# Optimization experiments

Measured on AMD Instinct MI355X. Metric: run time of the kernel, lower is better.

The kernel has to match this reference:

```python
import jax, jax.numpy as jnp
import numpy as np
import math

B, N, D = 4096, 41, 271
S, THR, KS = 0.3, 1e-4, 25  # wavelet scale s=0.3, threshold 1e-4, Bessel series terms
_IV_COEFS = [np.array([1.0 / (math.factorial(k) * math.factorial(k + n)) for k in range(KS)], dtype=np.float32) for n in range(4)]


def _iv(n, x):
    # modified Bessel I_n(x) via power series, x >= 0, shape [B]
    k = np.arange(KS, dtype=np.float32)
    xh = (0.5 * x)[:, None]
    return jnp.sum(_IV_COEFS[n] * xh ** (n + 2.0 * k), axis=-1)


def _l1norm(W):
    # F.normalize(p=1, dim=2)
    return W / jnp.maximum(jnp.sum(jnp.abs(W), axis=2, keepdims=True), 1e-12)


def _bn(x, g, b):
    # BatchNorm1d in training mode: per-feature stats over the batch dim (biased var)
    m = jnp.mean(x, 0)
    v = jnp.var(x, 0)
    return (x - m) / jnp.sqrt(v + 1e-5) * g + b


def _wavelet_basis(G):
    # laplacian_multi: degree from raw W, symmetrize, D^-1/2 (D - A) D^-1/2
    deg = jnp.sum(G, axis=-1)                               # [B,N]
    A = 0.5 * (G + jnp.swapaxes(G, 1, 2))                   # [B,N,N]
    dinv = 1.0 / (jnp.sqrt(deg) + 1e-6)
    eye = jnp.eye(N, dtype=G.dtype)
    L = dinv[:, :, None] * (deg[:, :, None] * eye - A) * dinv[:, None, :]
    # cheb_polynomial_multi: note order-0 term is ZEROS in the source
    T2 = 2.0 * jnp.matmul(L, L)
    T3 = 2.0 * jnp.matmul(L, T2) - L
    Lch = jnp.stack([jnp.zeros_like(L), L, T2, T3], axis=1)  # [B,4,N,N]
    # largest_lamb: host-side eigsh(LM) per sample -> detached (no grad)
    lam = jax.lax.stop_gradient(jnp.max(jnp.abs(jnp.linalg.eigvalsh(L)), axis=-1))  # [B]
    x = S * 0.5 * lam                                       # s * a, a = lamb/2
    ivs = jnp.stack([_iv(n, x) for n in range(4)], axis=1)  # [B,4]
    sign = jnp.asarray([1.0, -1.0, 1.0, -1.0], dtype=x.dtype)  # I_n(-x) = (-1)^n I_n(x)
    c = 2.0 * jnp.exp(x)[:, None] * ivs                     # 2 e^{sa} I_n(sa)
    inv_c = 2.0 * jnp.exp(-x)[:, None] * ivs * sign         # 2 e^{-sa} I_n(-sa)
    W = jnp.einsum('bo,bonm->bnm', c, Lch)
    Wi = jnp.einsum('bo,bonm->bnm', inv_c, Lch)
    W = _l1norm(jnp.where(W < THR, 0.0, W))
    Wi = _l1norm(jnp.where(Wi < THR, 0.0, Wi))
    return W, Wi


def _forward(G, X, gwnn_kernel, gwnn_W, log_scale_vector, W1, b1, W2, b2, bn1_gamma, bn1_beta):
    wav, wav_inv = _wavelet_basis(G)
    # graph wavelet layer: psi diag(k) psi^{-1} X W  (dropout off / eval)
    h = jnp.matmul(X, gwnn_W)                 # [B,N,D]
    h = jnp.matmul(wav_inv, h)
    h = gwnn_kernel[None, :, None] * h
    h = jax.nn.relu(jnp.matmul(wav, h))
    # scaling layer: exp(log_scale) * x
    coff = jnp.exp(log_scale_vector)          # [N,D]
    fr = coff[None] * h
    # shape1: Linear -> ReLU -> Linear
    fr = jnp.matmul(jax.nn.relu(jnp.matmul(fr, W1) + b1), W2) + b2
    # sequence feature: mean over nodes then BatchNorm1d(271)
    seq = _bn(jnp.mean(fr, axis=1), bn1_gamma, bn1_beta)  # [B,D]
    return seq


def setup_inputs() -> dict:
    key = jax.random.key(0)
    ks = jax.random.split(key, 8)
    sc = 1.0 / np.sqrt(D).astype(np.float32)
    return {
        'G': jax.random.uniform(ks[0], (B, N, N), jnp.float32),
        'X': jax.random.normal(ks[1], (B, N, D), jnp.float32),
        'gwnn_kernel': 1.0 + 0.1 * jax.random.normal(ks[2], (N,), jnp.float32),
        'gwnn_W': sc * jax.random.normal(ks[3], (D, D), jnp.float32),
        'log_scale_vector': 0.1 * jax.random.normal(ks[4], (N, D), jnp.float32),
        'W1': sc * jax.random.normal(ks[5], (D, D), jnp.float32),
        'b1': jnp.zeros((D,), jnp.float32),
        'W2': sc * jax.random.normal(ks[6], (D, D), jnp.float32),
        'b2': jnp.zeros((D,), jnp.float32),
        'bn1_gamma': jnp.ones((D,), jnp.float32),
        'bn1_beta': jnp.zeros((D,), jnp.float32),
    }


def reference(G, X, gwnn_kernel, gwnn_W, log_scale_vector, W1, b1, W2, b2, bn1_gamma, bn1_beta):
    return _forward(G, X, gwnn_kernel, gwnn_W, log_scale_vector, W1, b1, W2, b2, bn1_gamma, bn1_beta)
```

## Files before the change

kernel.cpp:

```cpp
#include <hip/hip_runtime.h>
#include <math.h>

namespace {
constexpr int BB = 4096;
constexpr int NN = 41;
constexpr int DD = 271;
constexpr int DP = 288;
constexpr int PW = 44;
constexpr long long MROWS = (long long)BB * NN;
constexpr int WBE = DP * DP * 2;
constexpr int WBS = (DP / 32) * DP * 32;
constexpr int SROW = 312;
constexpr int NPL = 5;
}

typedef __attribute__((ext_vector_type(8)))  unsigned short ushort8;
typedef __attribute__((ext_vector_type(8)))  short          short8;
typedef __attribute__((ext_vector_type(4)))  float          f32x4;

__device__ __forceinline__ unsigned short f2bf(float f) {
    unsigned u = __float_as_uint(f);
    unsigned r = (u + 0x7FFFu + ((u >> 16) & 1u)) >> 16;
    return (unsigned short)r;
}
__device__ __forceinline__ float bf2f(unsigned short h) {
    return __uint_as_float(((unsigned)h) << 16);
}

__device__ __forceinline__ void store_split_km(unsigned short* __restrict__ dst,
                                               long long nrows, long long row,
                                               int col, float v)
{
    const unsigned short hh = f2bf(v);
    const unsigned short ll = f2bf(v - bf2f(hh));
    const long long base = ((long long)(col >> 5) * nrows + row) * 64;
    const int cn = (col & 31) >> 3, k7 = col & 7, sw = (int)(row & 7);
    dst[base + ((cn ^ sw) << 3) + k7]       = hh;
    dst[base + (((cn + 4) ^ sw) << 3) + k7] = ll;
}

__device__ __forceinline__ void lds_mm(const float (*__restrict__ A)[PW],
                                       const float (*__restrict__ B)[PW],
                                       float (*__restrict__ C)[PW],
                                       const float scale,
                                       const float (*__restrict__ sub)[PW],
                                       const int tid)
{
    for (int s = tid; s < NN * 11; s += 256) {
        const int i = s / 11, q = s % 11;
        float4 acc = make_float4(0.f, 0.f, 0.f, 0.f);
        #pragma unroll
        for (int k = 0; k < NN; ++k) {
            const float a = A[i][k];
            const float4 b4 = *reinterpret_cast<const float4*>(&B[k][q * 4]);
            acc.x = fmaf(a, b4.x, acc.x); acc.y = fmaf(a, b4.y, acc.y);
            acc.z = fmaf(a, b4.z, acc.z); acc.w = fmaf(a, b4.w, acc.w);
        }
        float4 r;
        if (sub) {
            const float4 s4 = *reinterpret_cast<const float4*>(&sub[i][q * 4]);
            r = make_float4(fmaf(scale, acc.x, -s4.x), fmaf(scale, acc.y, -s4.y),
                            fmaf(scale, acc.z, -s4.z), fmaf(scale, acc.w, -s4.w));
        } else {
            r = make_float4(scale * acc.x, scale * acc.y, scale * acc.z, scale * acc.w);
        }
        *reinterpret_cast<float4*>(&C[i][q * 4]) = r;
    }
}

__global__ __launch_bounds__(256) void k_wavelet(const float* __restrict__ G,
                                                 const float* __restrict__ gk,
                                                 float* __restrict__ MT)
{
    __shared__ float sG[NN][PW];
    __shared__ float sL[NN][PW];
    __shared__ float sT2[NN][PW];
    __shared__ float sT3[NN][PW];
    __shared__ float sM[NN][PW];
    __shared__ float sdeg[NN], sdinv[NN], srs[NN];
    __shared__ float slam16;

    const int b   = blockIdx.x;
    const int tid = threadIdx.x;
    const float* Gb = G + (size_t)b * NN * NN;

    for (int e = tid; e < NN * PW; e += 256) {
        const int i = e / PW, j = e % PW;
        sG[i][j] = (j < NN) ? Gb[i * NN + j] : 0.0f;
    }
    __syncthreads();

    if (tid < NN) {
        float4 s4 = make_float4(0.f, 0.f, 0.f, 0.f);
        #pragma unroll
        for (int q = 0; q < 11; ++q) {
            const float4 g4 = *reinterpret_cast<const float4*>(&sG[tid][q * 4]);
            s4.x += g4.x; s4.y += g4.y; s4.z += g4.z; s4.w += g4.w;
        }
        const float s = (s4.x + s4.y) + (s4.z + s4.w);
        sdeg[tid]  = s;
        sdinv[tid] = 1.0f / (sqrtf(s) + 1e-6f);
    }
    __syncthreads();

    for (int e = tid; e < NN * PW; e += 256) {
        const int i = e / PW, j = e % PW;
        if (j < NN) {
            const float a = 0.5f * (sG[i][j] + sG[j][i]);
            const float v = ((i == j) ? sdeg[i] : 0.0f) - a;
            sL[i][j] = sdinv[i] * sdinv[j] * v;
        } else {
            sL[i][j] = 0.0f;
        }
    }
    __syncthreads();

    lds_mm(sL, sL, sT2, 2.0f, nullptr, tid);
    __syncthreads();
    lds_mm(sL, sT2, sT3, 2.0f, sL, tid);
    __syncthreads();

    lds_mm(sT2, sT2, sM, 0.25f, nullptr, tid);
    __syncthreads();
    lds_mm(sM, sM, sG, 1.0f, nullptr, tid);
    __syncthreads();
    lds_mm(sG, sG, sM, 1.0f, nullptr, tid);
    __syncthreads();

    if (tid < 64) {
        float lr[NN];
        #pragma unroll
        for (int j = 0; j < NN; ++j) lr[j] = (tid < NN) ? sM[tid][j] : 0.0f;
        unsigned h = (unsigned)(tid + 1) * 2654435761u;
        h ^= h >> 13; h *= 0x85ebca6bu; h ^= h >> 16;
        float v = (tid < NN) ? (0.25f + (float)(h & 1023) * (1.0f / 1024.0f)) : 0.0f;
        float n2 = v * v;
        #pragma unroll
        for (int off = 32; off > 0; off >>= 1) n2 += __shfl_xor(n2, off, 64);
        v *= rsqrtf(n2);
        float lam = 1.0f;
        #pragma unroll
        for (int it = 0; it < 4; ++it) {
            float acc = 0.f;
            #pragma unroll
            for (int j = 0; j < NN; ++j) acc = fmaf(lr[j], __shfl(v, j, 64), acc);
            float m2 = acc * acc;
            #pragma unroll
            for (int off = 32; off > 0; off >>= 1) m2 += __shfl_xor(m2, off, 64);
            lam = sqrtf(m2);
            v = acc * (1.0f / lam);
        }
        if (tid == 0) slam16 = lam;
    }
    __syncthreads();

    const float x = 0.15f * exp2f(log2f(slam16) * (1.0f / 16.0f));
    float iv[4];
    {
        const float xh = 0.5f * x, xh2 = xh * xh;
        #pragma unroll
        for (int n = 0; n < 4; ++n) {
            float c = 1.0f;
            for (int q = 2; q <= n; ++q) c /= (float)q;
            float p = 1.0f;
            for (int q = 0; q < n; ++q) p *= xh;
            float s = 0.f;
            for (int k = 0; k < 25; ++k) {
                s += c * p;
                p *= xh2;
                c /= (float)((k + 1) * (k + 1 + n));
            }
            iv[n] = s;
        }
    }
    const float ex = expf(x), emx = expf(-x);

    {
        const float a1 = 2.f * ex * iv[1], a2 = 2.f * ex * iv[2], a3 = 2.f * ex * iv[3];
        for (int s = tid; s < NN * 11; s += 256) {
            const int i = s / 11, q = s % 11;
            const float4 l4  = *reinterpret_cast<const float4*>(&sL[i][q * 4]);
            const float4 t24 = *reinterpret_cast<const float4*>(&sT2[i][q * 4]);
            const float4 t34 = *reinterpret_cast<const float4*>(&sT3[i][q * 4]);
            float4 w;
            w.x = fmaf(a1, l4.x, fmaf(a2, t24.x, a3 * t34.x));
            w.y = fmaf(a1, l4.y, fmaf(a2, t24.y, a3 * t34.y));
            w.z = fmaf(a1, l4.z, fmaf(a2, t24.z, a3 * t34.z));
            w.w = fmaf(a1, l4.w, fmaf(a2, t24.w, a3 * t34.w));
            w.x = (w.x < 1e-4f) ? 0.f : w.x;  w.y = (w.y < 1e-4f) ? 0.f : w.y;
            w.z = (w.z < 1e-4f) ? 0.f : w.z;  w.w = (w.w < 1e-4f) ? 0.f : w.w;
            *reinterpret_cast<float4*>(&sM[i][q * 4]) = w;
        }
        __syncthreads();
        if (tid < NN) {
            float s = 0.f;
            #pragma unroll
            for (int q = 0; q < 11; ++q) {
                const float4 w4 = *reinterpret_cast<const float4*>(&sM[tid][q * 4]);
                s += fabsf(w4.x) + fabsf(w4.y) + fabsf(w4.z) + fabsf(w4.w);
            }
            srs[tid] = 1.0f / fmaxf(s, 1e-12f);
        }
        __syncthreads();
    }
    {
        const float a1 = -2.f * emx * iv[1], a2 = 2.f * emx * iv[2], a3 = -2.f * emx * iv[3];
        for (int s = tid; s < NN * 11; s += 256) {
            const int i = s / 11, q = s % 11;
            float4 m4 = *reinterpret_cast<float4*>(&sM[i][q * 4]);
            const float rs = srs[i];
            m4.x *= rs; m4.y *= rs; m4.z *= rs; m4.w *= rs;
            *reinterpret_cast<float4*>(&sM[i][q * 4]) = m4;
            const float4 l4  = *reinterpret_cast<const float4*>(&sL[i][q * 4]);
            const float4 t24 = *reinterpret_cast<const float4*>(&sT2[i][q * 4]);
            const float4 t34 = *reinterpret_cast<const float4*>(&sT3[i][q * 4]);
            float4 w;
            w.x = fmaf(a1, l4.x, fmaf(a2, t24.x, a3 * t34.x));
            w.y = fmaf(a1, l4.y, fmaf(a2, t24.y, a3 * t34.y));
            w.z = fmaf(a1, l4.z, fmaf(a2, t24.z, a3 * t34.z));
            w.w = fmaf(a1, l4.w, fmaf(a2, t24.w, a3 * t34.w));
            w.x = (w.x < 1e-4f) ? 0.f : w.x;  w.y = (w.y < 1e-4f) ? 0.f : w.y;
            w.z = (w.z < 1e-4f) ? 0.f : w.z;  w.w = (w.w < 1e-4f) ? 0.f : w.w;
            *reinterpret_cast<float4*>(&sG[i][q * 4]) = w;
        }
        __syncthreads();
        if (tid < NN) {
            float s = 0.f;
            #pragma unroll
            for (int q = 0; q < 11; ++q) {
                const float4 w4 = *reinterpret_cast<const float4*>(&sG[tid][q * 4]);
                s += fabsf(w4.x) + fabsf(w4.y) + fabsf(w4.z) + fabsf(w4.w);
            }
            sdeg[tid] = gk[tid] / fmaxf(s, 1e-12f);
        }
        __syncthreads();
        for (int s = tid; s < NN * 11; s += 256) {
            const int j = s / 11, q = s % 11;
            float4 w4 = *reinterpret_cast<float4*>(&sG[j][q * 4]);
            const float rs = sdeg[j];
            w4.x *= rs; w4.y *= rs; w4.z *= rs; w4.w *= rs;
            *reinterpret_cast<float4*>(&sG[j][q * 4]) = w4;
        }
        __syncthreads();
    }
    lds_mm(sM, sG, sL, 1.0f, nullptr, tid);
    __syncthreads();
    float* dst = MT + (size_t)b * NN * NN;
    for (int e = tid; e < NN * NN; e += 256) {
        const int j = e / NN, i = e % NN;
        dst[e] = sL[i][j];
    }
}

__global__ __launch_bounds__(256) void k_splitB(const float* __restrict__ gW,
                                                const float* __restrict__ W1,
                                                const float* __restrict__ W2,
                                                const float* __restrict__ lsv,
                                                unsigned short* __restrict__ Bint,
                                                unsigned short* __restrict__ Bsng,
                                                float* __restrict__ coff)
{
    const int t = blockIdx.x * 256 + threadIdx.x;
    if (t < NN * DD) coff[t] = expf(lsv[t]);
    if (t >= 3 * DP * DP) return;
    const int w = t / (DP * DP);
    const int r = t % (DP * DP);
    const int n = r / DP, k = r % DP;
    const float* src = (w == 0) ? gW : ((w == 1) ? W1 : W2);
    const float v = (n < DD && k < DD) ? src[k * DD + n] : 0.0f;
    store_split_km(Bint + (size_t)w * WBE, DP, n, k, v);
    if (w < 2) {
        Bsng[(size_t)w * WBS + ((long long)(k >> 5) * DP + n) * 32 +
             (((k & 31) >> 3) << 3) + (k & 7)] = f2bf(v);
    }
}

__global__ __launch_bounds__(256, 2) void k_wavX(const float* __restrict__ MT,
                                                 const float* __restrict__ X,
                                                 unsigned short* __restrict__ Yint)
{
    constexpr int XJ  = 68;
    constexpr int YST = 296;
    __shared__ __align__(16) unsigned short sXT[288 * XJ];
    __shared__ __align__(16) unsigned short sMm[48 * XJ];
    __shared__ __align__(16) unsigned short sYb[NN * YST];
    const int b   = blockIdx.x;
    const int tid = threadIdx.x;
    const int lane = tid & 63, w = tid >> 6;
    const int lr = lane & 15;
    const int hi8 = (lane >> 4) * 8;

    const ushort8 z8 = {0, 0, 0, 0, 0, 0, 0, 0};
    for (int e = tid; e < (288 * XJ) / 8; e += 256)
        *reinterpret_cast<ushort8*>(&sXT[e * 8]) = z8;
    for (int e = tid; e < (48 * XJ) / 8; e += 256)
        *reinterpret_cast<ushort8*>(&sMm[e * 8]) = z8;
    __syncthreads();

    const float* __restrict__ Xb = X + (size_t)b * NN * DD;
    for (int e = tid; e < NN * DD; e += 256) {
        const int j = e / DD, c = e % DD;
        sXT[c * XJ + j] = f2bf(Xb[e]);
    }
    const float* __restrict__ Mb = MT + (size_t)b * NN * NN;
    for (int e = tid; e < NN * NN; e += 256) {
        const int j = e / NN, i = e % NN;
        sMm[i * XJ + j] = f2bf(Mb[e]);
    }
    __syncthreads();

    for (int t = w; t < 54; t += 4) {
        const int mt = t / 18, nt = t % 18;
        f32x4 acc = (f32x4){0.f, 0.f, 0.f, 0.f};
        #pragma unroll
        for (int ks = 0; ks < 2; ++ks) {
            const short8 a = *reinterpret_cast<const short8*>(
                &sMm[(mt * 16 + lr) * XJ + ks * 32 + hi8]);
            const short8 bf = *reinterpret_cast<const short8*>(
                &sXT[(nt * 16 + lr) * XJ + ks * 32 + hi8]);
            acc = __builtin_amdgcn_mfma_f32_16x16x32_bf16(a, bf, acc, 0, 0, 0);
        }
        const int row0 = mt * 16 + (lane >> 4) * 4;
        const int col  = nt * 16 + lr;
        #pragma unroll
        for (int rr = 0; rr < 4; ++rr) {
            const int row = row0 + rr;
            if (row < NN) sYb[row * YST + col] = f2bf(acc[rr]);
        }
    }
    __syncthreads();

    for (int t = tid; t < NN * 36; t += 256) {
        const int i = t / 36, c8 = t % 36;
        const ushort8 hv = *reinterpret_cast<const ushort8*>(&sYb[i * YST + c8 * 8]);
        const long long r = (long long)b * NN + i;
        const int p = c8 >> 3;
        const int chunk = ((c8 >> 2) & 1) * 4 + (c8 & 3);
        const int sw = (int)(r & 7);
        unsigned short* base = Yint + ((long long)p * MROWS + r) * 64;
        *reinterpret_cast<ushort8*>(base + ((chunk ^ sw) << 3)) = hv;
    }
}

__device__ __forceinline__ void async16(const unsigned short* __restrict__ g,
                                        unsigned short* l)
{
    __builtin_amdgcn_global_load_lds(
        (const __attribute__((address_space(1))) unsigned int*)g,
        (__attribute__((address_space(3))) unsigned int*)l, 16, 0, 0);
}

__global__ __launch_bounds__(512, 2) void k_fused(
    const unsigned short* __restrict__ Aint,
    const unsigned short* __restrict__ Bs0,
    const unsigned short* __restrict__ Bs1,
    const float* __restrict__ coff,
    const float* __restrict__ b1,
    float* __restrict__ seqsum)
{
    __shared__ __align__(16) unsigned short sS[256 * SROW];
    const int tid  = threadIdx.x;
    const int lane = tid & 63, w = tid >> 6;
    const int wr = w >> 1, wc = w & 1;
    const int lr = lane & 15, cb = lane >> 4;
    const int sw = lr & 7;

    const int nwg = gridDim.x, orig = blockIdx.x;
    const int q = nwg >> 3, r = nwg & 7;
    const int xcd = orig & 7, loc = orig >> 3;
    const int bid = (xcd < r ? xcd * (q + 1) : r * (q + 1) + (xcd - r) * q) + loc;
    const long long row0 = (long long)bid * 256;

    const unsigned short* __restrict__ b0p = Bs0 + (size_t)(wc * 144 + lr) * 32 + cb * 8;
    const unsigned short* __restrict__ b1p = Bs1 + (size_t)(wc * 144 + lr) * 32 + cb * 8;

    f32x4 acc[4][9];
    #pragma unroll
    for (int mf = 0; mf < 4; ++mf)
        #pragma unroll
        for (int nf = 0; nf < 9; ++nf)
            acc[mf][nf] = (f32x4){0.f, 0.f, 0.f, 0.f};

    for (int t = 0; t < 9; ++t) {
        const int p  = t >> 1;
        const int hc = (t & 1) * 4 + cb;
        const long long abase = ((long long)p * MROWS + row0) * 64 + ((hc ^ sw) << 3);
        short8 a[4];
        #pragma unroll
        for (int mf = 0; mf < 4; ++mf)
            a[mf] = *reinterpret_cast<const short8*>(
                Aint + abase + (long long)(wr * 64 + mf * 16 + lr) * 64);
        const long long toff = (long long)t * DP * 32;
        #pragma unroll
        for (int nf = 0; nf < 9; ++nf) {
            const short8 bh = *reinterpret_cast<const short8*>(b0p + toff + (long long)nf * 512);
            #pragma unroll
            for (int mf = 0; mf < 4; ++mf)
                acc[mf][nf] = __builtin_amdgcn_mfma_f32_16x16x32_bf16(a[mf], bh, acc[mf][nf], 0, 0, 0);
        }
    }

    #pragma unroll
    for (int mf = 0; mf < 4; ++mf) {
        const int mb = wr * 64 + mf * 16 + ((lane >> 4) * 4);
        #pragma unroll
        for (int nf = 0; nf < 9; ++nf) {
            const int col = wc * 144 + nf * 16 + lr;
            #pragma unroll
            for (int rr = 0; rr < 4; ++rr) {
                const int m = mb + rr;
                float v = fmaxf(acc[mf][nf][rr], 0.f);
                const float cf = (col < DD) ? coff[((unsigned)(row0 + m) % 41u) * DD + col] : 0.0f;
                sS[m * SROW + col] = f2bf(v * cf);
                acc[mf][nf][rr] = 0.f;
            }
        }
    }
    __syncthreads();

    for (int t = 0; t < 9; ++t) {
        short8 ah[4];
        #pragma unroll
        for (int mf = 0; mf < 4; ++mf) {
            const int m = wr * 64 + mf * 16 + lr;
            ah[mf] = *reinterpret_cast<const short8*>(&sS[m * SROW + t * 32 + cb * 8]);
        }
        const long long toff = (long long)t * DP * 32;
        #pragma unroll
        for (int nf = 0; nf < 9; ++nf) {
            const short8 bh = *reinterpret_cast<const short8*>(b1p + toff + (long long)nf * 512);
            #pragma unroll
            for (int mf = 0; mf < 4; ++mf)
                acc[mf][nf] = __builtin_amdgcn_mfma_f32_16x16x32_bf16(ah[mf], bh, acc[mf][nf], 0, 0, 0);
        }
    }
    __syncthreads();

    #pragma unroll
    for (int mf = 0; mf < 4; ++mf) {
        const int mb = wr * 64 + mf * 16 + ((lane >> 4) * 4);
        #pragma unroll
        for (int nf = 0; nf < 9; ++nf) {
            const int col = wc * 144 + nf * 16 + lr;
            const float bv = (col < DD) ? b1[col] : 0.0f;
            #pragma unroll
            for (int rr = 0; rr < 4; ++rr) {
                const float v = fmaxf(acc[mf][nf][rr] + bv, 0.f);
                sS[(mb + rr) * SROW + col] = f2bf(v);
            }
        }
    }
    __syncthreads();

    const long long b0 = row0 / 41;
    for (int e = tid; e < 8 * DP; e += 512) {
        const int ls = e / DP, col = e % DP;
        const long long bsm = b0 + ls;
        if (bsm >= BB) continue;
        const long long gr0 = bsm * 41, gr1 = gr0 + 41;
        const int m0 = (int)((gr0 > row0 ? gr0 : row0) - row0);
        const long long hi = (gr1 < row0 + 256 ? gr1 : row0 + 256);
        const int m1 = (int)(hi - row0);
        if (m0 >= m1) continue;
        float s = 0.f;
        for (int m = m0; m < m1; ++m) s += bf2f(sS[m * SROW + col]);
        atomicAdd(&seqsum[bsm * DP + col], s);
    }
}

__global__ __launch_bounds__(320) void k_mp(const float* __restrict__ seqsum,
                                            unsigned short* __restrict__ MPint)
{
    const int b = blockIdx.x;
    const int c = threadIdx.x;
    if (c >= DP) return;
    store_split_km(MPint, BB, b, c, seqsum[(size_t)b * DP + c] * (1.0f / 41.0f));
}

__global__ __launch_bounds__(256, 2) void k_gemm3(
    const unsigned short* __restrict__ Aint,
    const unsigned short* __restrict__ Bm,
    const float* __restrict__ bias,
    float* __restrict__ outF)
{
    __shared__ __align__(16) unsigned short As2[2][128 * 64];
    const int tid  = threadIdx.x;
    const int lane = tid & 63, w = tid >> 6;
    const int wr = w >> 1, wc = w & 1;
    const int lr = lane & 15, cb = lane >> 4;
    const int sw = lr & 7;
    const long long row0 = (long long)blockIdx.x * 128;

    const size_t brow = (size_t)(wc * 144 + lr) * 64;
    const unsigned short* __restrict__ bhp = Bm + brow + ((cb ^ sw) << 3);
    const unsigned short* __restrict__ blp = Bm + brow + (((cb + 4) ^ sw) << 3);

    f32x4 acc[4][9];
    #pragma unroll
    for (int mf = 0; mf < 4; ++mf)
        #pragma unroll
        for (int nf = 0; nf < 9; ++nf)
            acc[mf][nf] = (f32x4){0.f, 0.f, 0.f, 0.f};

    auto stageA = [&](unsigned short* dst, int kt32) {
        const unsigned short* src = Aint + ((long long)kt32 * BB + row0) * 64;
        #pragma unroll
        for (int i = 0; i < 4; ++i) {
            const int cid = tid + i * 256;
            async16(src + (long long)cid * 8, dst + cid * 8);
        }
    };

    stageA(As2[0], 0);
    for (int t = 0; t < 9; ++t) {
        __syncthreads();
        if (t < 8) stageA(As2[(t + 1) & 1], t + 1);
        const unsigned short* As = As2[t & 1];
        short8 ah[4], al[4];
        #pragma unroll
        for (int mf = 0; mf < 4; ++mf) {
            const int m = wr * 64 + mf * 16 + lr;
            ah[mf] = *reinterpret_cast<const short8*>(&As[m * 64 + ((cb ^ sw) << 3)]);
            al[mf] = *reinterpret_cast<const short8*>(&As[m * 64 + (((cb + 4) ^ sw) << 3)]);
        }
        const long long toff = (long long)t * DP * 64;
        #pragma unroll
        for (int nf = 0; nf < 9; ++nf) {
            const long long d = toff + (long long)nf * 1024;
            const short8 bh = *reinterpret_cast<const short8*>(bhp + d);
            const short8 bl = *reinterpret_cast<const short8*>(blp + d);
            #pragma unroll
            for (int mf = 0; mf < 4; ++mf) {
                acc[mf][nf] = __builtin_amdgcn_mfma_f32_16x16x32_bf16(ah[mf], bh, acc[mf][nf], 0, 0, 0);
                acc[mf][nf] = __builtin_amdgcn_mfma_f32_16x16x32_bf16(al[mf], bh, acc[mf][nf], 0, 0, 0);
                acc[mf][nf] = __builtin_amdgcn_mfma_f32_16x16x32_bf16(ah[mf], bl, acc[mf][nf], 0, 0, 0);
            }
        }
    }

    #pragma unroll
    for (int mf = 0; mf < 4; ++mf) {
        const long long rb = row0 + wr * 64 + mf * 16 + ((lane >> 4) * 4);
        #pragma unroll
        for (int nf = 0; nf < 9; ++nf) {
            const int col = wc * 144 + nf * 16 + lr;
            const float bv = (col < DD) ? bias[col] : 0.0f;
            #pragma unroll
            for (int rr = 0; rr < 4; ++rr)
                outF[(rb + rr) * DP + col] = acc[mf][nf][rr] + bv;
        }
    }
}

__global__ __launch_bounds__(256) void k_stats(const float* __restrict__ seq, float* __restrict__ stats)
{
    __shared__ float s1[256], s2[256];
    const int d = blockIdx.x;
    float a = 0.f, q = 0.f;
    for (int b = threadIdx.x; b < BB; b += 256) {
        float v = seq[(size_t)b * DP + d];
        a += v; q = fmaf(v, v, q);
    }
    s1[threadIdx.x] = a; s2[threadIdx.x] = q;
    __syncthreads();
    for (int o = 128; o > 0; o >>= 1) {
        if (threadIdx.x < o) { s1[threadIdx.x] += s1[threadIdx.x + o]; s2[threadIdx.x] += s2[threadIdx.x + o]; }
        __syncthreads();
    }
    if (threadIdx.x == 0) {
        float m = s1[0] * (1.0f / BB);
        float v = s2[0] * (1.0f / BB) - m * m;
        stats[d]      = m;
        stats[DD + d] = 1.0f / sqrtf(v + 1e-5f);
    }
}

__global__ __launch_bounds__(256) void k_bn(const float* __restrict__ seq, const float* __restrict__ stats,
                                            const float* __restrict__ g, const float* __restrict__ bt,
                                            float* __restrict__ out)
{
    const long long idx = (long long)blockIdx.x * 256 + threadIdx.x;
    if (idx < (long long)BB * DD) {
        const int d = (int)(idx % DD);
        const long long b = idx / DD;
        out[idx] = (seq[b * DP + d] - stats[d]) * stats[DD + d] * g[d] + bt[d];
    }
}

extern "C" void kernel_launch(void* const* d_in, const int* in_sizes, int n_in,
                              void* d_out, int out_size, void* d_ws, size_t ws_size,
                              hipStream_t stream)
{
    const float* G   = (const float*)d_in[0];
    const float* X   = (const float*)d_in[1];
    const float* gk  = (const float*)d_in[2];
    const float* gW  = (const float*)d_in[3];
    const float* lsv = (const float*)d_in[4];
    const float* W1  = (const float*)d_in[5];
    const float* b1  = (const float*)d_in[6];
    const float* W2  = (const float*)d_in[7];
    const float* b2  = (const float*)d_in[8];
    const float* gam = (const float*)d_in[9];
    const float* bet = (const float*)d_in[10];

    char* p = (char*)d_ws;
    auto alloc = [&](size_t bytes) { void* r = (void*)p; p += (bytes + 255) & ~(size_t)255; return r; };
    float*          MT     = (float*)alloc((size_t)BB * NN * NN * 4);
    unsigned short* Yint   = (unsigned short*)alloc((size_t)NPL * MROWS * 64 * 2);
    unsigned short* Bint   = (unsigned short*)alloc((size_t)3 * WBE * 2);
    unsigned short* Bsng   = (unsigned short*)alloc((size_t)2 * WBS * 2);
    unsigned short* MPint  = (unsigned short*)alloc((size_t)BB * 576 * 2);
    float*          coff   = (float*)alloc((size_t)NN * DD * 4);
    float*          seqsum = (float*)alloc((size_t)BB * DP * 4);
    float*          seqF   = (float*)alloc((size_t)BB * DP * 4);
    float*          stats  = (float*)alloc(2 * DD * 4);

    hipMemsetAsync(seqsum, 0, (size_t)BB * DP * 4, stream);

    k_wavelet<<<BB, 256, 0, stream>>>(G, gk, MT);
    k_splitB<<<(3 * DP * DP + 255) / 256, 256, 0, stream>>>(gW, W1, W2, lsv, Bint, Bsng, coff);
    k_wavX<<<BB, 256, 0, stream>>>(MT, X, Yint);

    k_fused<<<(unsigned)(MROWS / 256), 512, 0, stream>>>(Yint, Bsng, Bsng + WBS,
                                                         coff, b1, seqsum);
    k_mp<<<BB, 320, 0, stream>>>(seqsum, MPint);
    k_gemm3<<<BB / 128, 256, 0, stream>>>(MPint, Bint + 2 * WBE, b2, seqF);
    k_stats<<<DD, 256, 0, stream>>>(seqF, stats);
    k_bn<<<(unsigned)(((long long)BB * DD + 255) / 256), 256, 0, stream>>>(seqF, stats, gam, bet, (float*)d_out);
}
```

Baseline: 418.1 us.

## Fuse wavelet basis construction into wavelet-X matmul kernel via shared LDS union

Merges the per-sample wavelet basis kernel with the kernel that multiplies the basis by X, so the basis is handed over in LDS as bf16 instead of being written to and reread from a global MT buffer. The LDS scratch for the Laplacian and Chebyshev matrices is aliased with the X-transpose and output staging buffers. This removes one launch and the global MT traffic. The fused kernel needs more LDS per block and runs the eigen and Laplacian phase under tighter occupancy.

```diff
diff --git a/kernel.cpp b/kernel.cpp
--- a/kernel.cpp
+++ b/kernel.cpp
@@ -12,6 +12,7 @@
 constexpr int WBS = (DP / 32) * DP * 32;
 constexpr int SROW = 312;
 constexpr int NPL = 5;
+constexpr int MSZ = NN * PW * 4;
 }
 
 typedef __attribute__((ext_vector_type(8)))  unsigned short ushort8;
@@ -68,22 +69,33 @@
     }
 }
 
-__global__ __launch_bounds__(256) void k_wavelet(const float* __restrict__ G,
-                                                 const float* __restrict__ gk,
-                                                 float* __restrict__ MT)
-{
-    __shared__ float sG[NN][PW];
-    __shared__ float sL[NN][PW];
-    __shared__ float sT2[NN][PW];
-    __shared__ float sT3[NN][PW];
-    __shared__ float sM[NN][PW];
+__global__ __launch_bounds__(256, 2) void k_wav(const float* __restrict__ G,
+                                                const float* __restrict__ gk,
+                                                const float* __restrict__ X,
+                                                unsigned short* __restrict__ Yint)
+{
+    constexpr int XJ  = 68;
+    constexpr int YST = 296;
+    __shared__ __align__(16) char um[288 * XJ * 2 + NN * YST * 2];
+    __shared__ __align__(16) unsigned short sMm[48 * XJ];
     __shared__ float sdeg[NN], sdinv[NN], srs[NN];
     __shared__ float slam16;
+
+    float (*sG)[PW]  = reinterpret_cast<float(*)[PW]>(um + 0 * MSZ);
+    float (*sL)[PW]  = reinterpret_cast<float(*)[PW]>(um + 1 * MSZ);
+    float (*sT2)[PW] = reinterpret_cast<float(*)[PW]>(um + 2 * MSZ);
+    float (*sT3)[PW] = reinterpret_cast<float(*)[PW]>(um + 3 * MSZ);
+    float (*sM)[PW]  = reinterpret_cast<float(*)[PW]>(um + 4 * MSZ);
 
     const int b   = blockIdx.x;
     const int tid = threadIdx.x;
     const float* Gb = G + (size_t)b * NN * NN;
 
+    {
+        const ushort8 z8 = {0, 0, 0, 0, 0, 0, 0, 0};
+        for (int e = tid; e < (48 * XJ) / 8; e += 256)
+            *reinterpret_cast<ushort8*>(&sMm[e * 8]) = z8;
+    }
     for (int e = tid; e < NN * PW; e += 256) {
         const int i = e / PW, j = e % PW;
         sG[i][j] = (j < NN) ? Gb[i * NN + j] : 0.0f;
@@ -245,10 +257,63 @@
     }
     lds_mm(sM, sG, sL, 1.0f, nullptr, tid);
     __syncthreads();
-    float* dst = MT + (size_t)b * NN * NN;
+
     for (int e = tid; e < NN * NN; e += 256) {
-        const int j = e / NN, i = e % NN;
-        dst[e] = sL[i][j];
+        const int i = e / NN, j = e % NN;
+        sMm[i * XJ + j] = f2bf(sL[i][j]);
+    }
+    __syncthreads();
+
+    unsigned short* sXT = reinterpret_cast<unsigned short*>(um);
+    unsigned short* sYb = reinterpret_cast<unsigned short*>(um + 288 * XJ * 2);
+    const int lane = tid & 63, w = tid >> 6;
+    const int lr = lane & 15;
+    const int hi8 = (lane >> 4) * 8;
+
+    {
+        const ushort8 z8 = {0, 0, 0, 0, 0, 0, 0, 0};
+        for (int e = tid; e < (288 * XJ) / 8; e += 256)
+            *reinterpret_cast<ushort8*>(&sXT[e * 8]) = z8;
+    }
+    __syncthreads();
+
+    const float* __restrict__ Xb = X + (size_t)b * NN * DD;
+    for (int e = tid; e < NN * DD; e += 256) {
+        const int j = e / DD, c = e % DD;
+        sXT[c * XJ + j] = f2bf(Xb[e]);
+    }
+    __syncthreads();
+
+    for (int t = w; t < 54; t += 4) {
+        const int mt = t / 18, nt = t % 18;
+        f32x4 acc = (f32x4){0.f, 0.f, 0.f, 0.f};
+        #pragma unroll
+        for (int ks = 0; ks < 2; ++ks) {
+            const short8 a = *reinterpret_cast<const short8*>(
+                &sMm[(mt * 16 + lr) * XJ + ks * 32 + hi8]);
+            const short8 bf = *reinterpret_cast<const short8*>(
+                &sXT[(nt * 16 + lr) * XJ + ks * 32 + hi8]);
+            acc = __builtin_amdgcn_mfma_f32_16x16x32_bf16(a, bf, acc, 0, 0, 0);
+        }
+        const int row0 = mt * 16 + (lane >> 4) * 4;
+        const int col  = nt * 16 + lr;
+        #pragma unroll
+        for (int rr = 0; rr < 4; ++rr) {
+            const int row = row0 + rr;
+            if (row < NN) sYb[row * YST + col] = f2bf(acc[rr]);
+        }
+    }
+    __syncthreads();
+
+    for (int t = tid; t < NN * 36; t += 256) {
+        const int i = t / 36, c8 = t % 36;
+        const ushort8 hv = *reinterpret_cast<const ushort8*>(&sYb[i * YST + c8 * 8]);
+        const long long r = (long long)b * NN + i;
+        const int p = c8 >> 3;
+        const int chunk = ((c8 >> 2) & 1) * 4 + (c8 & 3);
+        const int sw = (int)(r & 7);
+        unsigned short* base = Yint + ((long long)p * MROWS + r) * 64;
+        *reinterpret_cast<ushort8*>(base + ((chunk ^ sw) << 3)) = hv;
     }
 }
 
@@ -272,73 +337,6 @@
     if (w < 2) {
         Bsng[(size_t)w * WBS + ((long long)(k >> 5) * DP + n) * 32 +
              (((k & 31) >> 3) << 3) + (k & 7)] = f2bf(v);
-    }
-}
-
-__global__ __launch_bounds__(256, 2) void k_wavX(const float* __restrict__ MT,
-                                                 const float* __restrict__ X,
-                                                 unsigned short* __restrict__ Yint)
-{
-    constexpr int XJ  = 68;
-    constexpr int YST = 296;
-    __shared__ __align__(16) unsigned short sXT[288 * XJ];
-    __shared__ __align__(16) unsigned short sMm[48 * XJ];
-    __shared__ __align__(16) unsigned short sYb[NN * YST];
-    const int b   = blockIdx.x;
-    const int tid = threadIdx.x;
-    const int lane = tid & 63, w = tid >> 6;
-    const int lr = lane & 15;
-    const int hi8 = (lane >> 4) * 8;
-
-    const ushort8 z8 = {0, 0, 0, 0, 0, 0, 0, 0};
-    for (int e = tid; e < (288 * XJ) / 8; e += 256)
-        *reinterpret_cast<ushort8*>(&sXT[e * 8]) = z8;
-    for (int e = tid; e < (48 * XJ) / 8; e += 256)
-        *reinterpret_cast<ushort8*>(&sMm[e * 8]) = z8;
-    __syncthreads();
-
-    const float* __restrict__ Xb = X + (size_t)b * NN * DD;
-    for (int e = tid; e < NN * DD; e += 256) {
-        const int j = e / DD, c = e % DD;
-        sXT[c * XJ + j] = f2bf(Xb[e]);
-    }
-    const float* __restrict__ Mb = MT + (size_t)b * NN * NN;
-    for (int e = tid; e < NN * NN; e += 256) {
-        const int j = e / NN, i = e % NN;
-        sMm[i * XJ + j] = f2bf(Mb[e]);
-    }
-    __syncthreads();
-
-    for (int t = w; t < 54; t += 4) {
-        const int mt = t / 18, nt = t % 18;
-        f32x4 acc = (f32x4){0.f, 0.f, 0.f, 0.f};
-        #pragma unroll
-        for (int ks = 0; ks < 2; ++ks) {
-            const short8 a = *reinterpret_cast<const short8*>(
-                &sMm[(mt * 16 + lr) * XJ + ks * 32 + hi8]);
-            const short8 bf = *reinterpret_cast<const short8*>(
-                &sXT[(nt * 16 + lr) * XJ + ks * 32 + hi8]);
-            acc = __builtin_amdgcn_mfma_f32_16x16x32_bf16(a, bf, acc, 0, 0, 0);
-        }
-        const int row0 = mt * 16 + (lane >> 4) * 4;
-        const int col  = nt * 16 + lr;
-        #pragma unroll
-        for (int rr = 0; rr < 4; ++rr) {
-            const int row = row0 + rr;
-            if (row < NN) sYb[row * YST + col] = f2bf(acc[rr]);
-        }
-    }
-    __syncthreads();
-
-    for (int t = tid; t < NN * 36; t += 256) {
-        const int i = t / 36, c8 = t % 36;
-        const ushort8 hv = *reinterpret_cast<const ushort8*>(&sYb[i * YST + c8 * 8]);
-        const long long r = (long long)b * NN + i;
-        const int p = c8 >> 3;
-        const int chunk = ((c8 >> 2) & 1) * 4 + (c8 & 3);
-        const int sw = (int)(r & 7);
-        unsigned short* base = Yint + ((long long)p * MROWS + r) * 64;
-        *reinterpret_cast<ushort8*>(base + ((chunk ^ sw) << 3)) = hv;
     }
 }
 
@@ -605,7 +603,6 @@
 
     char* p = (char*)d_ws;
     auto alloc = [&](size_t bytes) { void* r = (void*)p; p += (bytes + 255) & ~(size_t)255; return r; };
-    float*          MT     = (float*)alloc((size_t)BB * NN * NN * 4);
     unsigned short* Yint   = (unsigned short*)alloc((size_t)NPL * MROWS * 64 * 2);
     unsigned short* Bint   = (unsigned short*)alloc((size_t)3 * WBE * 2);
     unsigned short* Bsng   = (unsigned short*)alloc((size_t)2 * WBS * 2);
@@ -617,9 +614,8 @@
 
     hipMemsetAsync(seqsum, 0, (size_t)BB * DP * 4, stream);
 
-    k_wavelet<<<BB, 256, 0, stream>>>(G, gk, MT);
     k_splitB<<<(3 * DP * DP + 255) / 256, 256, 0, stream>>>(gW, W1, W2, lsv, Bint, Bsng, coff);
-    k_wavX<<<BB, 256, 0, stream>>>(MT, X, Yint);
+    k_wav<<<BB, 256, 0, stream>>>(G, gk, X, Yint);
 
     k_fused<<<(unsigned)(MROWS / 256), 512, 0, stream>>>(Yint, Bsng, Bsng + WBS,
                                                          coff, b1, seqsum);
```

Measured after the change: 467.0 us. 11.7% more time.
